# Performance work log

Hardware: AMD Instinct MI355X
Metric: run time of the kernel (lower is better)

## Reference

```python
import jax, jax.numpy as jnp
import numpy as np

NUM_HEADS = 2
NUM_POINTS = 8
EMBED_DIM = 128


def conv2d(x, w, b, pad):
    # x: [B,C,H,W], w: [O,I,kh,kw]
    y = jax.lax.conv_general_dilated(
        x, w, window_strides=(1, 1), padding=[(pad, pad), (pad, pad)],
        dimension_numbers=('NCHW', 'OIHW', 'NCHW'))
    return y + b[None, :, None, None]


def grid_sample_bilinear(img, g):
    # img: [C,H,W]; g: [Ho,Wo,2] in [-1,1], (x, y) order; align_corners=False, zero padding
    C, H, W = img.shape
    x = ((g[..., 0] + 1.0) * W - 1.0) * 0.5
    y = ((g[..., 1] + 1.0) * H - 1.0) * 0.5
    x0 = jnp.floor(x); y0 = jnp.floor(y)
    x1 = x0 + 1.0; y1 = y0 + 1.0
    wx = x - x0; wy = y - y0

    def gather(yi, xi):
        valid = (xi >= 0) & (xi < W) & (yi >= 0) & (yi < H)
        xi_c = jnp.clip(xi, 0, W - 1).astype(jnp.int32)
        yi_c = jnp.clip(yi, 0, H - 1).astype(jnp.int32)
        v = img[:, yi_c, xi_c]  # [C,Ho,Wo]
        return v * valid[None].astype(img.dtype)

    out = (gather(y0, x0) * ((1 - wy) * (1 - wx))[None]
           + gather(y0, x1) * ((1 - wy) * wx)[None]
           + gather(y1, x0) * (wy * (1 - wx))[None]
           + gather(y1, x1) * (wy * wx)[None])
    return out  # [C,Ho,Wo]


def setup_inputs() -> dict:
    key = jax.random.key(0)
    ks = jax.random.split(key, 6)
    B, C, H, W = 8, EMBED_DIM, 96, 96
    query = jax.random.normal(ks[0], (B, C, H, W), dtype=jnp.float32)
    value = jax.random.normal(ks[1], (B, C, H, W), dtype=jnp.float32)
    reference_points = jax.random.uniform(ks[2], (B, H, W, NUM_HEADS, NUM_POINTS, 2), dtype=jnp.float32)
    attn_w = jax.random.normal(ks[3], (NUM_HEADS * NUM_POINTS, C, 3, 3), dtype=jnp.float32) * 0.05
    attn_b = jnp.zeros((NUM_HEADS * NUM_POINTS,), dtype=jnp.float32)
    proj_w = jax.random.normal(ks[4], (C, C, 1, 1), dtype=jnp.float32) * 0.05
    proj_b = jnp.zeros((C,), dtype=jnp.float32)
    return {"query": query, "value": value, "reference_points": reference_points,
            "attn_w": attn_w, "attn_b": attn_b, "proj_w": proj_w, "proj_b": proj_b}


def reference(query, value, reference_points, attn_w, attn_b, proj_w, proj_b):
    B, C, H, W = query.shape
    nh, npts = NUM_HEADS, NUM_POINTS
    hd = C // nh

    # attention weights: Conv2d(C, nh*np, 3, pad=1) -> softmax over points
    attn = conv2d(query, attn_w, attn_b, 1).reshape(B, nh, npts, H, W)
    attn = jax.nn.softmax(attn, axis=2)

    # grid: [B,H,W,nh,np,2] in [0,1] -> [-1,1] -> [B*nh, np, H, W, 2]
    grid = reference_points * 2.0 - 1.0
    grid = jnp.transpose(grid, (0, 3, 4, 1, 2, 5)).reshape(B * nh, npts, H, W, 2)

    # value per head: [B*nh, hd, H, W]
    val = value.reshape(B, nh, hd, H, W).reshape(B * nh, hd, H, W)

    # sample each point from the shared per-head value map (no materialized expand)
    sample_pts = jax.vmap(grid_sample_bilinear, in_axes=(None, 0))   # over points
    sampled = jax.vmap(sample_pts, in_axes=(0, 0))(val, grid)        # [B*nh, np, hd, H, W]
    sampled = sampled.reshape(B, nh, npts, hd, H, W)

    # weighted sum over points
    weighted = jnp.einsum('bnphw,bnpdhw->bndhw', attn, sampled).reshape(B, C, H, W)

    return conv2d(weighted, proj_w, proj_b, 0)
```

## Files before the change

### kernel.cpp

```cpp
#include <hip/hip_runtime.h>
#include <hip/hip_bf16.h>

#define BB 8
#define CC 128
#define HH 96
#define WW 96
#define HWH (HH*WW)
#define NH 2
#define NP 8
#define PW 98
#define PHW (PW*PW)

typedef __attribute__((ext_vector_type(8))) short short8;
typedef __attribute__((ext_vector_type(4))) float f32x4;

__device__ __forceinline__ float bf_lo(unsigned u) { return __uint_as_float(u << 16); }
__device__ __forceinline__ float bf_hi(unsigned u) { return __uint_as_float(u & 0xffff0000u); }

__global__ __launch_bounds__(256) void prep_w_kernel(
    const float* __restrict__ aw, const float* __restrict__ pw,
    __hip_bfloat16* __restrict__ wtb, __hip_bfloat16* __restrict__ pwb) {
  int t = blockIdx.x * 256 + threadIdx.x;
  for (int idx = t; idx < 9 * 16 * 16 * 8; idx += gridDim.x * 256) {
    int j = idx & 7;
    int o = (idx >> 3) & 15;
    int g = (idx >> 7) & 15;
    int k = idx >> 11;
    int c = g * 8 + j;
    wtb[idx] = __float2bfloat16(aw[o * 1152 + c * 9 + k]);
  }
  for (int idx = t; idx < 128 * 128; idx += gridDim.x * 256) {
    pwb[idx] = __float2bfloat16(pw[idx]);
  }
}

__global__ __launch_bounds__(256) void transpose_cl_kernel(
    const float* __restrict__ value, const float* __restrict__ query,
    __hip_bfloat16* __restrict__ val_t, __hip_bfloat16* __restrict__ q_pad) {
  __shared__ float tile[64][65];
  int blk = blockIdx.x;
  int mode = blk / 2304;
  int r = blk % 2304;
  int ptile = r % 144;
  int bn = r / 144;
  int b = bn >> 1, n = bn & 1;
  int pix0 = ptile * 64;
  int t = threadIdx.x;
  int lane = t & 63;
  int row4 = t >> 6;

  const float* srcp = (mode ? query : value) + ((size_t)(b * CC + n * 64)) * HWH + pix0;
#pragma unroll
  for (int i = 0; i < 16; ++i) {
    int c = i * 4 + row4;
    tile[c][lane] = srcp[(size_t)c * HWH + lane];
  }
  __syncthreads();

  int d2 = t & 31;
  int ph = t >> 5;
  if (mode == 0) {
    __hip_bfloat16* dst = val_t + ((size_t)bn * HWH + pix0) * 64;
#pragma unroll
    for (int i = 0; i < 8; ++i) {
      int p = i * 8 + ph;
      __hip_bfloat162 v;
      v.x = __float2bfloat16(tile[d2 * 2][p]);
      v.y = __float2bfloat16(tile[d2 * 2 + 1][p]);
      *reinterpret_cast<__hip_bfloat162*>(dst + (size_t)p * 64 + d2 * 2) = v;
    }
  } else {
#pragma unroll
    for (int i = 0; i < 8; ++i) {
      int p = i * 8 + ph;
      int gp = pix0 + p;
      int h = gp / WW, w = gp - h * WW;
      __hip_bfloat162 v;
      v.x = __float2bfloat16(tile[d2 * 2][p]);
      v.y = __float2bfloat16(tile[d2 * 2 + 1][p]);
      size_t off = ((size_t)b * PHW + (size_t)(h + 1) * PW + (w + 1)) * 128 + n * 64 + d2 * 2;
      *reinterpret_cast<__hip_bfloat162*>(q_pad + off) = v;
    }
  }
}

__global__ __launch_bounds__(256) void attn_conv_mfma2(
    const __hip_bfloat16* __restrict__ q_pad, const __hip_bfloat16* __restrict__ wtb_,
    const float* __restrict__ bias, float* __restrict__ attn_out) {
  int t = threadIdx.x;
  int l = t & 63;
  int bid = blockIdx.x;
  int sbid = (bid & 7) * 144 + (bid >> 3);
  int tid = __builtin_amdgcn_readfirstlane(sbid * 4 + (t >> 6));
  int b = tid / 576;
  int rem = tid % 576;
  int h = rem / 6;
  int w0 = (rem % 6) * 16;

  const char* qb = (const char*)q_pad;
  const char* wb = (const char*)wtb_;

  int pxbase = b * PHW + (h + 1) * PW + (w0 + 1);
  int lb  = (l & 15) * 256 + (l >> 4) * 16;
  int wlb = (l >> 4) * 256 + (l & 15) * 16;

  float bias_o = bias[l & 15];
  f32x4 acc0 = {bias_o, bias_o, bias_o, bias_o};
  f32x4 acc1 = {0.f, 0.f, 0.f, 0.f};

#pragma unroll
  for (int k = 0; k < 9; ++k) {
    int dy = k / 3 - 1, dx = (k % 3) - 1;
    const char* abase = qb + ((size_t)pxbase + dy * PW + dx) * 256 + lb;
    const char* bbase = wb + k * 4096 + wlb;
#pragma unroll
    for (int c4 = 0; c4 < 4; ++c4) {
      short8 a = *(const short8*)(abase + c4 * 64);
      short8 bf = *(const short8*)(bbase + c4 * 1024);
      if (k & 1)
        acc1 = __builtin_amdgcn_mfma_f32_16x16x32_bf16(a, bf, acc1, 0, 0, 0);
      else
        acc0 = __builtin_amdgcn_mfma_f32_16x16x32_bf16(a, bf, acc0, 0, 0, 0);
    }
  }

  int o = l & 15;
  size_t row0 = (size_t)b * HWH + (size_t)h * 96 + w0 + (l >> 4) * 4;
#pragma unroll
  for (int r = 0; r < 4; ++r) {
    float vv = acc0[r] + acc1[r];
    float mx = vv;
    mx = fmaxf(mx, __shfl_xor(mx, 1, 64));
    mx = fmaxf(mx, __shfl_xor(mx, 2, 64));
    mx = fmaxf(mx, __shfl_xor(mx, 4, 64));
    float e = __expf(vv - mx);
    float s = e;
    s += __shfl_xor(s, 1, 64);
    s += __shfl_xor(s, 2, 64);
    s += __shfl_xor(s, 4, 64);
    attn_out[(row0 + r) * 16 + o] = e / s;
  }
}

__global__ __launch_bounds__(256) void sample_kernel(
    const __hip_bfloat16* __restrict__ val_t, const float* __restrict__ attn,
    const float* __restrict__ refp, __hip_bfloat16* __restrict__ weighted) {
  int t = threadIdx.x;
  int lane = t & 63;
  int sub = lane >> 4;
  int lq = lane & 15;
  int bid = blockIdx.x;
  int sbid = (bid & 7) * 1152 + (bid >> 3);
  int unit = (sbid * 4 + (t >> 6)) * 4 + sub;
  int bn = unit / HWH;
  int pix = unit - bn * HWH;
  int bq = bn >> 1, n = bn & 1;

  const float* ap = attn + ((size_t)bq * HWH + pix) * 16 + n * 8;
  const float* rp = refp + (((size_t)bq * HWH + pix) * NH + n) * 16;
  const __hip_bfloat16* vb = val_t + (size_t)bn * (HWH * 64);

  float4 a0 = *(const float4*)(ap);
  float4 a1 = *(const float4*)(ap + 4);
  float4 r0 = *(const float4*)(rp);
  float4 r1 = *(const float4*)(rp + 4);
  float4 r2 = *(const float4*)(rp + 8);
  float4 r3 = *(const float4*)(rp + 12);
  float aa[8] = {a0.x, a0.y, a0.z, a0.w, a1.x, a1.y, a1.z, a1.w};
  float rr[16] = {r0.x, r0.y, r0.z, r0.w, r1.x, r1.y, r1.z, r1.w,
                  r2.x, r2.y, r2.z, r2.w, r3.x, r3.y, r3.z, r3.w};

  float acc0 = 0.f, acc1 = 0.f, acc2 = 0.f, acc3 = 0.f;
  int lq4 = lq * 4;
#pragma unroll
  for (int p = 0; p < 8; ++p) {
    float a = aa[p];
    float x = rr[p * 2 + 0] * (float)WW - 0.5f;
    float y = rr[p * 2 + 1] * (float)HH - 0.5f;
    float x0f = floorf(x), y0f = floorf(y);
    float wx = x - x0f, wy = y - y0f;
    int x0 = (int)x0f, y0 = (int)y0f;

    float ay0 = a * (1.f - wy);  ay0 = (y0 >= 0)      ? ay0 : 0.f;
    float ay1 = a * wy;          ay1 = (y0 < HH - 1)  ? ay1 : 0.f;
    float bx0 = 1.f - wx;        bx0 = (x0 >= 0)      ? bx0 : 0.f;
    float bx1 = wx;              bx1 = (x0 < WW - 1)  ? bx1 : 0.f;

    int xc0 = max(x0, 0), xc1 = min(x0 + 1, WW - 1);
    int yc0 = max(y0, 0), yc1 = min(y0 + 1, HH - 1);

    int r0o = yc0 * (WW * 64);
    int r1o = yc1 * (WW * 64);
    int c0o = xc0 * 64 + lq4;
    int c1o = xc1 * 64 + lq4;

    uint2 u00 = *(const uint2*)(vb + (r0o + c0o));
    uint2 u01 = *(const uint2*)(vb + (r0o + c1o));
    uint2 u10 = *(const uint2*)(vb + (r1o + c0o));
    uint2 u11 = *(const uint2*)(vb + (r1o + c1o));

    float w00 = ay0 * bx0, w01 = ay0 * bx1, w10 = ay1 * bx0, w11 = ay1 * bx1;

    acc0 = fmaf(bf_lo(u00.x), w00, acc0);
    acc1 = fmaf(bf_hi(u00.x), w00, acc1);
    acc2 = fmaf(bf_lo(u00.y), w00, acc2);
    acc3 = fmaf(bf_hi(u00.y), w00, acc3);

    acc0 = fmaf(bf_lo(u01.x), w01, acc0);
    acc1 = fmaf(bf_hi(u01.x), w01, acc1);
    acc2 = fmaf(bf_lo(u01.y), w01, acc2);
    acc3 = fmaf(bf_hi(u01.y), w01, acc3);

    acc0 = fmaf(bf_lo(u10.x), w10, acc0);
    acc1 = fmaf(bf_hi(u10.x), w10, acc1);
    acc2 = fmaf(bf_lo(u10.y), w10, acc2);
    acc3 = fmaf(bf_hi(u10.y), w10, acc3);

    acc0 = fmaf(bf_lo(u11.x), w11, acc0);
    acc1 = fmaf(bf_hi(u11.x), w11, acc1);
    acc2 = fmaf(bf_lo(u11.y), w11, acc2);
    acc3 = fmaf(bf_hi(u11.y), w11, acc3);
  }

  ushort4 outv;
  __hip_bfloat16 h0 = __float2bfloat16(acc0);
  __hip_bfloat16 h1 = __float2bfloat16(acc1);
  __hip_bfloat16 h2 = __float2bfloat16(acc2);
  __hip_bfloat16 h3 = __float2bfloat16(acc3);
  outv.x = *(unsigned short*)&h0;
  outv.y = *(unsigned short*)&h1;
  outv.z = *(unsigned short*)&h2;
  outv.w = *(unsigned short*)&h3;
  *(ushort4*)(weighted + ((size_t)bq * HWH + pix) * 128 + n * 64 + lq4) = outv;
}

__global__ __launch_bounds__(256) void proj_mfma_kernel(
    const __hip_bfloat16* __restrict__ weighted, const __hip_bfloat16* __restrict__ pwb,
    const float* __restrict__ pb, float* __restrict__ out) {
  int t = threadIdx.x;
  int l = t & 63;
  int wv = t >> 6;
  int px0 = (blockIdx.x * 4 + wv) * 16;
  int b = px0 / HWH;
  int pixl0 = px0 - b * HWH;

  const short* wgt = (const short*)pwb;
  const short* act = (const short*)weighted;

  short8 bfrag[4];
#pragma unroll
  for (int kk = 0; kk < 4; ++kk)
    bfrag[kk] = *(const short8*)(act + ((size_t)(px0 + (l & 15)) << 7) + kk * 32 + (l >> 4) * 8);

  int arow = (l & 15) << 7;
  int kofs = (l >> 4) * 8;

  float* ob0 = out + (size_t)b * CC * HWH + pixl0 + (l & 15);
  int corow = (l >> 4) * 4;

#pragma unroll 2
  for (int ct = 0; ct < 8; ++ct) {
    float4 pb4 = *(const float4*)(pb + ct * 16 + corow);
    f32x4 acc = {pb4.x, pb4.y, pb4.z, pb4.w};
#pragma unroll
    for (int kk = 0; kk < 4; ++kk) {
      short8 afrag = *(const short8*)(wgt + ((ct * 16) << 7) + arow + kk * 32 + kofs);
      acc = __builtin_amdgcn_mfma_f32_16x16x32_bf16(afrag, bfrag[kk], acc, 0, 0, 0);
    }
    float* obc = ob0 + (size_t)(ct * 16 + corow) * HWH;
#pragma unroll
    for (int r = 0; r < 4; ++r)
      obc[(size_t)r * HWH] = acc[r];
  }
}

extern "C" void kernel_launch(void* const* d_in, const int* in_sizes, int n_in,
                              void* d_out, int out_size, void* d_ws, size_t ws_size,
                              hipStream_t stream) {
  const float* query = (const float*)d_in[0];
  const float* value = (const float*)d_in[1];
  const float* refp  = (const float*)d_in[2];
  const float* aw    = (const float*)d_in[3];
  const float* ab    = (const float*)d_in[4];
  const float* pw    = (const float*)d_in[5];
  const float* pb    = (const float*)d_in[6];
  float* out = (float*)d_out;

  char* ws = (char*)d_ws;
  __hip_bfloat16* wtb      = (__hip_bfloat16*)(ws);
  __hip_bfloat16* pwb      = (__hip_bfloat16*)(ws + 40960);
  float* attn_sm           = (float*)(ws + 73728);
  __hip_bfloat16* val_t    = (__hip_bfloat16*)(ws + 4792320);
  __hip_bfloat16* q_pad    = (__hip_bfloat16*)(ws + 23666688);
  __hip_bfloat16* weighted = (__hip_bfloat16*)(ws + 23666688);

  hipMemsetAsync(q_pad, 0, (size_t)BB * PHW * 128 * 2, stream);
  prep_w_kernel<<<72, 256, 0, stream>>>(aw, pw, wtb, pwb);
  transpose_cl_kernel<<<4608, 256, 0, stream>>>(value, query, val_t, q_pad);
  attn_conv_mfma2<<<1152, 256, 0, stream>>>(q_pad, wtb, ab, attn_sm);
  sample_kernel<<<9216, 256, 0, stream>>>(val_t, attn_sm, refp, weighted);
  proj_mfma_kernel<<<(BB * HWH) / 64, 256, 0, stream>>>(weighted, pwb, pb, out);
}
```

Measured before the change: 234.7 us.

## Fuse bilinear sampling with projection GEMM through swizzled LDS tile

Merges the sampling kernel and the 1x1 projection MFMA kernel into one kernel. Each block samples 64 pixels for both heads, writes the bf16 weighted values into an XOR-swizzled shared-memory tile, then runs the projection from LDS. This removes the global round trip of the weighted intermediate and one kernel launch. The accumulation also switches to packed two-wide float FMAs. In exchange there are fewer blocks (1152 instead of 9216), each doing more serial sampling work, which can reduce the latency hiding available for the gathers.

```diff
diff --git a/kernel.cpp b/kernel.cpp
--- a/kernel.cpp
+++ b/kernel.cpp
@@ -13,6 +13,7 @@
 
 typedef __attribute__((ext_vector_type(8))) short short8;
 typedef __attribute__((ext_vector_type(4))) float f32x4;
+typedef __attribute__((ext_vector_type(2))) float f32x2;
 
 __device__ __forceinline__ float bf_lo(unsigned u) { return __uint_as_float(u << 16); }
 __device__ __forceinline__ float bf_hi(unsigned u) { return __uint_as_float(u & 0xffff0000u); }
@@ -142,121 +143,121 @@
   }
 }
 
-__global__ __launch_bounds__(256) void sample_kernel(
+__global__ __launch_bounds__(256) void fused_sp_kernel(
     const __hip_bfloat16* __restrict__ val_t, const float* __restrict__ attn,
-    const float* __restrict__ refp, __hip_bfloat16* __restrict__ weighted) {
-  int t = threadIdx.x;
-  int lane = t & 63;
-  int sub = lane >> 4;
-  int lq = lane & 15;
-  int bid = blockIdx.x;
-  int sbid = (bid & 7) * 1152 + (bid >> 3);
-  int unit = (sbid * 4 + (t >> 6)) * 4 + sub;
-  int bn = unit / HWH;
-  int pix = unit - bn * HWH;
-  int bq = bn >> 1, n = bn & 1;
-
-  const float* ap = attn + ((size_t)bq * HWH + pix) * 16 + n * 8;
-  const float* rp = refp + (((size_t)bq * HWH + pix) * NH + n) * 16;
-  const __hip_bfloat16* vb = val_t + (size_t)bn * (HWH * 64);
-
-  float4 a0 = *(const float4*)(ap);
-  float4 a1 = *(const float4*)(ap + 4);
-  float4 r0 = *(const float4*)(rp);
-  float4 r1 = *(const float4*)(rp + 4);
-  float4 r2 = *(const float4*)(rp + 8);
-  float4 r3 = *(const float4*)(rp + 12);
-  float aa[8] = {a0.x, a0.y, a0.z, a0.w, a1.x, a1.y, a1.z, a1.w};
-  float rr[16] = {r0.x, r0.y, r0.z, r0.w, r1.x, r1.y, r1.z, r1.w,
-                  r2.x, r2.y, r2.z, r2.w, r3.x, r3.y, r3.z, r3.w};
-
-  float acc0 = 0.f, acc1 = 0.f, acc2 = 0.f, acc3 = 0.f;
-  int lq4 = lq * 4;
-#pragma unroll
-  for (int p = 0; p < 8; ++p) {
-    float a = aa[p];
-    float x = rr[p * 2 + 0] * (float)WW - 0.5f;
-    float y = rr[p * 2 + 1] * (float)HH - 0.5f;
-    float x0f = floorf(x), y0f = floorf(y);
-    float wx = x - x0f, wy = y - y0f;
-    int x0 = (int)x0f, y0 = (int)y0f;
-
-    float ay0 = a * (1.f - wy);  ay0 = (y0 >= 0)      ? ay0 : 0.f;
-    float ay1 = a * wy;          ay1 = (y0 < HH - 1)  ? ay1 : 0.f;
-    float bx0 = 1.f - wx;        bx0 = (x0 >= 0)      ? bx0 : 0.f;
-    float bx1 = wx;              bx1 = (x0 < WW - 1)  ? bx1 : 0.f;
-
-    int xc0 = max(x0, 0), xc1 = min(x0 + 1, WW - 1);
-    int yc0 = max(y0, 0), yc1 = min(y0 + 1, HH - 1);
-
-    int r0o = yc0 * (WW * 64);
-    int r1o = yc1 * (WW * 64);
-    int c0o = xc0 * 64 + lq4;
-    int c1o = xc1 * 64 + lq4;
-
-    uint2 u00 = *(const uint2*)(vb + (r0o + c0o));
-    uint2 u01 = *(const uint2*)(vb + (r0o + c1o));
-    uint2 u10 = *(const uint2*)(vb + (r1o + c0o));
-    uint2 u11 = *(const uint2*)(vb + (r1o + c1o));
-
-    float w00 = ay0 * bx0, w01 = ay0 * bx1, w10 = ay1 * bx0, w11 = ay1 * bx1;
-
-    acc0 = fmaf(bf_lo(u00.x), w00, acc0);
-    acc1 = fmaf(bf_hi(u00.x), w00, acc1);
-    acc2 = fmaf(bf_lo(u00.y), w00, acc2);
-    acc3 = fmaf(bf_hi(u00.y), w00, acc3);
-
-    acc0 = fmaf(bf_lo(u01.x), w01, acc0);
-    acc1 = fmaf(bf_hi(u01.x), w01, acc1);
-    acc2 = fmaf(bf_lo(u01.y), w01, acc2);
-    acc3 = fmaf(bf_hi(u01.y), w01, acc3);
-
-    acc0 = fmaf(bf_lo(u10.x), w10, acc0);
-    acc1 = fmaf(bf_hi(u10.x), w10, acc1);
-    acc2 = fmaf(bf_lo(u10.y), w10, acc2);
-    acc3 = fmaf(bf_hi(u10.y), w10, acc3);
-
-    acc0 = fmaf(bf_lo(u11.x), w11, acc0);
-    acc1 = fmaf(bf_hi(u11.x), w11, acc1);
-    acc2 = fmaf(bf_lo(u11.y), w11, acc2);
-    acc3 = fmaf(bf_hi(u11.y), w11, acc3);
-  }
-
-  ushort4 outv;
-  __hip_bfloat16 h0 = __float2bfloat16(acc0);
-  __hip_bfloat16 h1 = __float2bfloat16(acc1);
-  __hip_bfloat16 h2 = __float2bfloat16(acc2);
-  __hip_bfloat16 h3 = __float2bfloat16(acc3);
-  outv.x = *(unsigned short*)&h0;
-  outv.y = *(unsigned short*)&h1;
-  outv.z = *(unsigned short*)&h2;
-  outv.w = *(unsigned short*)&h3;
-  *(ushort4*)(weighted + ((size_t)bq * HWH + pix) * 128 + n * 64 + lq4) = outv;
-}
-
-__global__ __launch_bounds__(256) void proj_mfma_kernel(
-    const __hip_bfloat16* __restrict__ weighted, const __hip_bfloat16* __restrict__ pwb,
+    const float* __restrict__ refp, const __hip_bfloat16* __restrict__ pwb,
     const float* __restrict__ pb, float* __restrict__ out) {
+  __shared__ char lds[16384];
   int t = threadIdx.x;
   int l = t & 63;
   int wv = t >> 6;
-  int px0 = (blockIdx.x * 4 + wv) * 16;
-  int b = px0 / HWH;
-  int pixl0 = px0 - b * HWH;
-
+  int sub = l >> 4;
+  int lq = l & 15;
+  int lq8 = lq * 8;
+
+  int bid = blockIdx.x;
+  int sbid = (bid & 7) * 144 + (bid >> 3);
+  int b = sbid / 144;
+  int px0l = (sbid % 144) * 64;
+  size_t gpx0 = (size_t)b * HWH + px0l;
+
+#pragma unroll 2
+  for (int i = 0; i < 8; ++i) {
+    int u = i * 16 + wv * 4 + sub;
+    int n = u & 1;
+    int pxl = u >> 1;
+    int pix = px0l + pxl;
+
+    const float* ap = attn + (gpx0 + pxl) * 16 + n * 8;
+    const float* rp = refp + ((gpx0 + pxl) * NH + n) * 16;
+    const __hip_bfloat16* vb = val_t + (size_t)(b * 2 + n) * (HWH * 64);
+
+    float4 a0 = *(const float4*)(ap);
+    float4 a1 = *(const float4*)(ap + 4);
+    float4 r0 = *(const float4*)(rp);
+    float4 r1 = *(const float4*)(rp + 4);
+    float4 r2 = *(const float4*)(rp + 8);
+    float4 r3 = *(const float4*)(rp + 12);
+    float aa[8] = {a0.x, a0.y, a0.z, a0.w, a1.x, a1.y, a1.z, a1.w};
+    float rr[16] = {r0.x, r0.y, r0.z, r0.w, r1.x, r1.y, r1.z, r1.w,
+                    r2.x, r2.y, r2.z, r2.w, r3.x, r3.y, r3.z, r3.w};
+
+    f32x2 acc01 = {0.f, 0.f}, acc23 = {0.f, 0.f};
+    int lq4 = lq * 4;
+#pragma unroll
+    for (int p = 0; p < 8; ++p) {
+      float a = aa[p];
+      float x = rr[p * 2 + 0] * (float)WW - 0.5f;
+      float y = rr[p * 2 + 1] * (float)HH - 0.5f;
+      float x0f = floorf(x), y0f = floorf(y);
+      float wx = x - x0f, wy = y - y0f;
+      int x0 = (int)x0f, y0 = (int)y0f;
+
+      float ay0 = a * (1.f - wy);  ay0 = (y0 >= 0)      ? ay0 : 0.f;
+      float ay1 = a * wy;          ay1 = (y0 < HH - 1)  ? ay1 : 0.f;
+      float bx0 = 1.f - wx;        bx0 = (x0 >= 0)      ? bx0 : 0.f;
+      float bx1 = wx;              bx1 = (x0 < WW - 1)  ? bx1 : 0.f;
+
+      int xc0 = max(x0, 0), xc1 = min(x0 + 1, WW - 1);
+      int yc0 = max(y0, 0), yc1 = min(y0 + 1, HH - 1);
+
+      int r0o = yc0 * (WW * 64);
+      int r1o = yc1 * (WW * 64);
+      int c0o = xc0 * 64 + lq4;
+      int c1o = xc1 * 64 + lq4;
+
+      uint2 u00 = *(const uint2*)(vb + (r0o + c0o));
+      uint2 u01 = *(const uint2*)(vb + (r0o + c1o));
+      uint2 u10 = *(const uint2*)(vb + (r1o + c0o));
+      uint2 u11 = *(const uint2*)(vb + (r1o + c1o));
+
+      float w00 = ay0 * bx0, w01 = ay0 * bx1, w10 = ay1 * bx0, w11 = ay1 * bx1;
+
+      f32x2 wv2;
+      wv2 = (f32x2){w00, w00};
+      acc01 = __builtin_elementwise_fma((f32x2){bf_lo(u00.x), bf_hi(u00.x)}, wv2, acc01);
+      acc23 = __builtin_elementwise_fma((f32x2){bf_lo(u00.y), bf_hi(u00.y)}, wv2, acc23);
+      wv2 = (f32x2){w01, w01};
+      acc01 = __builtin_elementwise_fma((f32x2){bf_lo(u01.x), bf_hi(u01.x)}, wv2, acc01);
+      acc23 = __builtin_elementwise_fma((f32x2){bf_lo(u01.y), bf_hi(u01.y)}, wv2, acc23);
+      wv2 = (f32x2){w10, w10};
+      acc01 = __builtin_elementwise_fma((f32x2){bf_lo(u10.x), bf_hi(u10.x)}, wv2, acc01);
+      acc23 = __builtin_elementwise_fma((f32x2){bf_lo(u10.y), bf_hi(u10.y)}, wv2, acc23);
+      wv2 = (f32x2){w11, w11};
+      acc01 = __builtin_elementwise_fma((f32x2){bf_lo(u11.x), bf_hi(u11.x)}, wv2, acc01);
+      acc23 = __builtin_elementwise_fma((f32x2){bf_lo(u11.y), bf_hi(u11.y)}, wv2, acc23);
+    }
+
+    ushort4 outv;
+    __hip_bfloat16 h0 = __float2bfloat16(acc01.x);
+    __hip_bfloat16 h1 = __float2bfloat16(acc01.y);
+    __hip_bfloat16 h2 = __float2bfloat16(acc23.x);
+    __hip_bfloat16 h3 = __float2bfloat16(acc23.y);
+    outv.x = *(unsigned short*)&h0;
+    outv.y = *(unsigned short*)&h1;
+    outv.z = *(unsigned short*)&h2;
+    outv.w = *(unsigned short*)&h3;
+    int byte = pxl * 256 + n * 128 + lq8;
+    byte ^= (pxl & 7) << 4;
+    *(ushort4*)(&lds[byte]) = outv;
+  }
+  __syncthreads();
+
+  int pxl_r = wv * 16 + (l & 15);
   const short* wgt = (const short*)pwb;
-  const short* act = (const short*)weighted;
 
   short8 bfrag[4];
 #pragma unroll
-  for (int kk = 0; kk < 4; ++kk)
-    bfrag[kk] = *(const short8*)(act + ((size_t)(px0 + (l & 15)) << 7) + kk * 32 + (l >> 4) * 8);
+  for (int kk = 0; kk < 4; ++kk) {
+    int byte = pxl_r * 256 + kk * 64 + (l >> 4) * 16;
+    byte ^= (pxl_r & 7) << 4;
+    bfrag[kk] = *(const short8*)(&lds[byte]);
+  }
 
   int arow = (l & 15) << 7;
   int kofs = (l >> 4) * 8;
-
-  float* ob0 = out + (size_t)b * CC * HWH + pixl0 + (l & 15);
   int corow = (l >> 4) * 4;
+  float* ob0 = out + (size_t)b * CC * HWH + (px0l + wv * 16) + (l & 15);
 
 #pragma unroll 2
   for (int ct = 0; ct < 8; ++ct) {
@@ -287,17 +288,15 @@
   float* out = (float*)d_out;
 
   char* ws = (char*)d_ws;
-  __hip_bfloat16* wtb      = (__hip_bfloat16*)(ws);
-  __hip_bfloat16* pwb      = (__hip_bfloat16*)(ws + 40960);
-  float* attn_sm           = (float*)(ws + 73728);
-  __hip_bfloat16* val_t    = (__hip_bfloat16*)(ws + 4792320);
-  __hip_bfloat16* q_pad    = (__hip_bfloat16*)(ws + 23666688);
-  __hip_bfloat16* weighted = (__hip_bfloat16*)(ws + 23666688);
+  __hip_bfloat16* wtb   = (__hip_bfloat16*)(ws);
+  __hip_bfloat16* pwb   = (__hip_bfloat16*)(ws + 40960);
+  float* attn_sm        = (float*)(ws + 73728);
+  __hip_bfloat16* val_t = (__hip_bfloat16*)(ws + 4792320);
+  __hip_bfloat16* q_pad = (__hip_bfloat16*)(ws + 23666688);
 
   hipMemsetAsync(q_pad, 0, (size_t)BB * PHW * 128 * 2, stream);
   prep_w_kernel<<<72, 256, 0, stream>>>(aw, pw, wtb, pwb);
   transpose_cl_kernel<<<4608, 256, 0, stream>>>(value, query, val_t, q_pad);
   attn_conv_mfma2<<<1152, 256, 0, stream>>>(q_pad, wtb, ab, attn_sm);
-  sample_kernel<<<9216, 256, 0, stream>>>(val_t, attn_sm, refp, weighted);
-  proj_mfma_kernel<<<(BB * HWH) / 64, 256, 0, stream>>>(weighted, pwb, pb, out);
-}
+  fused_sp_kernel<<<1152, 256, 0, stream>>>(val_t, attn_sm, refp, pwb, pb, out);
+}
```

Result: no change. 234.3 us (-0.2%).
